# Performance work log

Measured on AMD Instinct MI355X. Metric: run time of the kernel, lower is better.

Reference implementation:

```python
import jax, jax.numpy as jnp
import numpy as np

B, S, D, H = 2, 2048, 1024, 16  # batch, seq_len, d_model(=d_k=d_v), heads
HD = D // H                      # per-head dim = 64


def setup_inputs() -> dict:
    key = jax.random.key(0)
    ks = jax.random.split(key, 7)
    s = 0.02  # weight init scale
    return {
        "queries": jax.random.normal(ks[0], (B, S, D), dtype=jnp.float32),
        "keys":    jax.random.normal(ks[1], (B, S, D), dtype=jnp.float32),
        "values":  jax.random.normal(ks[2], (B, S, D), dtype=jnp.float32),
        "Wq": jax.random.normal(ks[3], (D, D), dtype=jnp.float32) * s,
        "bq": jnp.zeros((D,), dtype=jnp.float32),
        "Wk": jax.random.normal(ks[4], (D, D), dtype=jnp.float32) * s,
        "bk": jnp.zeros((D,), dtype=jnp.float32),
        "Wv": jax.random.normal(ks[5], (D, D), dtype=jnp.float32) * s,
        "bv": jnp.zeros((D,), dtype=jnp.float32),
        "Wo": jax.random.normal(ks[6], (D, D), dtype=jnp.float32) * s,
        "bo": jnp.zeros((D,), dtype=jnp.float32),
    }


def reference(queries, keys, values, Wq, bq, Wk, bk, Wv, bv, Wo, bo):
    def split_heads(x):  # [B,S,D] -> [B,H,S,HD]
        return x.reshape(B, S, H, HD).transpose(0, 2, 1, 3)

    q = split_heads(queries @ Wq + bq)
    k = split_heads(keys @ Wk + bk)
    v = split_heads(values @ Wv + bv)

    # NOTE: original module scales by sqrt(total d_k = D), not per-head dim.
    scores = jnp.einsum('bhqd,bhkd->bhqk', q, k) / jnp.sqrt(jnp.float32(D))
    weights = jax.nn.softmax(scores, axis=-1)
    o = jnp.einsum('bhqk,bhkd->bhqd', weights, v)

    o = o.transpose(0, 2, 1, 3).reshape(B, S, D)  # merge heads
    return o @ Wo + bo
```

## Files before the change

### kernel.cpp

```cpp
#include <hip/hip_runtime.h>
#include <hip/hip_bf16.h>
#include <stdint.h>

#define S_LEN 2048
#define D_MOD 1024
#define NHEAD 16
#define BATCH 2
#define M_TOT (BATCH * S_LEN)

typedef __bf16 bf16_t;
typedef __bf16 bf16x8 __attribute__((ext_vector_type(8)));
typedef __bf16 bf16x4 __attribute__((ext_vector_type(4)));
typedef float f32x4 __attribute__((ext_vector_type(4)));

typedef __attribute__((address_space(1))) void gas_void;
typedef __attribute__((address_space(3))) void las_void;

__device__ __forceinline__ void gload_lds16(const void* g, void* l) {
#if defined(__has_builtin) && __has_builtin(__builtin_amdgcn_global_load_lds)
  __builtin_amdgcn_global_load_lds((gas_void*)g, (las_void*)l, 16u, 0, 0u);
#else
  *(bf16x8*)l = *(const bf16x8*)g;
#endif
}

__device__ __forceinline__ f32x4 mfma16(bf16x8 a, bf16x8 b, f32x4 c) {
  return __builtin_amdgcn_mfma_f32_16x16x32_bf16(a, b, c, 0, 0, 0);
}

__global__ __launch_bounds__(256) void cvt3_kernel(
    const float* __restrict__ a, const float* __restrict__ b, const float* __restrict__ c,
    bf16_t* __restrict__ oa, bf16_t* __restrict__ ob, bf16_t* __restrict__ oc)
{
  const float* in  = blockIdx.z == 0 ? a : (blockIdx.z == 1 ? b : c);
  bf16_t*      out = blockIdx.z == 0 ? oa : (blockIdx.z == 1 ? ob : oc);
  int i = blockIdx.x * 256 + threadIdx.x;
  float4 v = ((const float4*)in)[i];
  bf16x4 o;
  o[0] = (bf16_t)v.x; o[1] = (bf16_t)v.y; o[2] = (bf16_t)v.z; o[3] = (bf16_t)v.w;
  ((bf16x4*)out)[i] = o;
}

__global__ __launch_bounds__(256) void wtrans_kernel(
    const float* __restrict__ w0, const float* __restrict__ w1,
    const float* __restrict__ w2, const float* __restrict__ w3,
    bf16_t* __restrict__ t0, bf16_t* __restrict__ t1,
    bf16_t* __restrict__ t2, bf16_t* __restrict__ t3)
{
  __shared__ float tile[64][65];
  const int z = blockIdx.z;
  const float* W = z == 0 ? w0 : (z == 1 ? w1 : (z == 2 ? w2 : w3));
  bf16_t* Wt     = z == 0 ? t0 : (z == 1 ? t1 : (z == 2 ? t2 : t3));
  const int tid = threadIdx.x;
  const int kb = blockIdx.y * 64, nb = blockIdx.x * 64;
#pragma unroll
  for (int j = 0; j < 16; j++) {
    int flat = j * 256 + tid;
    int kr = flat >> 6, nc = flat & 63;
    tile[kr][nc] = W[(size_t)(kb + kr) * D_MOD + nb + nc];
  }
  __syncthreads();
#pragma unroll
  for (int j = 0; j < 16; j++) {
    int flat = j * 256 + tid;
    int nr = flat >> 6, kc = flat & 63;
    Wt[(size_t)(nb + nr) * D_MOD + kb + kc] = (bf16_t)tile[kc][nr];
  }
}

__device__ __forceinline__ void gemm_core(const bf16_t* __restrict__ A,
                                          const bf16_t* __restrict__ Bt,
                                          bf16_t* As, bf16_t* Bs,
                                          int mbase, int nbase, f32x4 acc[4][4])
{
  const int tid = threadIdx.x;
  const int lane = tid & 63, wave = tid >> 6;
  const int lrow = lane & 15, lg = lane >> 4;
  const int wm = wave >> 1, wn = wave & 1;
  for (int kt = 0; kt < D_MOD; kt += 64) {
    __syncthreads();
#pragma unroll
    for (int j = 0; j < 4; j++) {
      int flat = j * 256 + tid;
      int r = flat >> 3, c8 = flat & 7;
      gload_lds16(A  + (size_t)(mbase + r) * D_MOD + kt + c8 * 8, As + flat * 8);
      gload_lds16(Bt + (size_t)(nbase + r) * D_MOD + kt + c8 * 8, Bs + flat * 8);
    }
    __syncthreads();
#pragma unroll
    for (int kc = 0; kc < 2; kc++) {
      bf16x8 af[4], bfr[4];
#pragma unroll
      for (int mt = 0; mt < 4; mt++)
        af[mt] = *(const bf16x8*)(As + (wm * 64 + mt * 16 + lrow) * 64 + kc * 32 + lg * 8);
#pragma unroll
      for (int nt = 0; nt < 4; nt++)
        bfr[nt] = *(const bf16x8*)(Bs + (wn * 64 + nt * 16 + lrow) * 64 + kc * 32 + lg * 8);
#pragma unroll
      for (int mt = 0; mt < 4; mt++)
#pragma unroll
        for (int nt = 0; nt < 4; nt++)
          acc[mt][nt] = mfma16(af[mt], bfr[nt], acc[mt][nt]);
    }
  }
}

__global__ __launch_bounds__(256) void gemm_qkv_kernel(
    const bf16_t* __restrict__ Xq, const bf16_t* __restrict__ Xk, const bf16_t* __restrict__ Xv,
    const bf16_t* __restrict__ WqT, const bf16_t* __restrict__ WkT, const bf16_t* __restrict__ WvT,
    const float* __restrict__ bq, const float* __restrict__ bk, const float* __restrict__ bv,
    bf16_t* __restrict__ Qp, bf16_t* __restrict__ Kp, bf16_t* __restrict__ Vt)
{
  __shared__ __align__(16) bf16_t As[128 * 64];
  __shared__ __align__(16) bf16_t Bs[128 * 64];
  const int z = blockIdx.z;
  const bf16_t* A    = z == 0 ? Xq  : (z == 1 ? Xk  : Xv);
  const bf16_t* Bt   = z == 0 ? WqT : (z == 1 ? WkT : WvT);
  const float*  bias = z == 0 ? bq  : (z == 1 ? bk  : bv);
  f32x4 acc[4][4] = {};
  const int mbase = blockIdx.y * 128, nbase = blockIdx.x * 128;
  gemm_core(A, Bt, As, Bs, mbase, nbase, acc);
  const int tid = threadIdx.x, lane = tid & 63, wave = tid >> 6;
  const int lrow = lane & 15, lg = lane >> 4, wm = wave >> 1, wn = wave & 1;
  if (z < 2) {
    bf16_t* Out = z == 0 ? Qp : Kp;
#pragma unroll
    for (int mt = 0; mt < 4; mt++) {
      int r0 = mbase + wm * 64 + mt * 16 + lg * 4;
#pragma unroll
      for (int nt = 0; nt < 4; nt++) {
        int col = nbase + wn * 64 + nt * 16 + lrow;
        float bb = bias[col];
#pragma unroll
        for (int r = 0; r < 4; r++)
          Out[(size_t)(r0 + r) * D_MOD + col] = (bf16_t)(acc[mt][nt][r] + bb);
      }
    }
  } else {
#pragma unroll
    for (int mt = 0; mt < 4; mt++) {
      int r0 = mbase + wm * 64 + mt * 16 + lg * 4;
      int b = r0 >> 11, s0 = r0 & (S_LEN - 1);
#pragma unroll
      for (int nt = 0; nt < 4; nt++) {
        int col = nbase + wn * 64 + nt * 16 + lrow;
        float bb = bias[col];
        bf16x4 pk;
#pragma unroll
        for (int r = 0; r < 4; r++) pk[r] = (bf16_t)(acc[mt][nt][r] + bb);
        *(bf16x4*)(Vt + ((size_t)(b * NHEAD + (col >> 6)) * 64 + (col & 63)) * S_LEN + s0) = pk;
      }
    }
  }
}

__global__ __launch_bounds__(256) void attn_kernel(
    const bf16_t* __restrict__ Q, const bf16_t* __restrict__ K,
    const bf16_t* __restrict__ Vt, bf16_t* __restrict__ O)
{
  __shared__ __align__(16) bf16_t Ks[2][64 * 64];
  __shared__ __align__(16) bf16_t Vs[2][64 * 64];
  __shared__ __align__(16) bf16_t plds[4][32 * 72];
  const int tid = threadIdx.x, wave = tid >> 6, lane = tid & 63;
  const int lrow = lane & 15, lg = lane >> 4;
  const int bh = blockIdx.y;
  const int b = bh >> 4, h = bh & 15;
  const int qbase = blockIdx.x * 128 + wave * 32;
  const bf16_t* Kb = K + (size_t)(b * S_LEN) * D_MOD + h * 64;
  const bf16_t* Vb = Vt + (size_t)bh * 64 * S_LEN;

  bf16x8 qf[2][2];
#pragma unroll
  for (int qr = 0; qr < 2; qr++) {
    const bf16_t* Qrow = Q + (size_t)(b * S_LEN + qbase + qr * 16 + lrow) * D_MOD + h * 64;
    qf[qr][0] = *(const bf16x8*)(Qrow + lg * 8);
    qf[qr][1] = *(const bf16x8*)(Qrow + 32 + lg * 8);
  }

  float mrow[2][4], lsum[2][4];
  f32x4 oacc[2][4] = {};
#pragma unroll
  for (int qr = 0; qr < 2; qr++)
#pragma unroll
    for (int r = 0; r < 4; r++) { mrow[qr][r] = -1e30f; lsum[qr][r] = 0.f; }

  bf16_t* pl = (bf16_t*)plds[wave];
  const float sc2 = 0.03125f * 1.44269504f;
  const int rs = lrow & 7;

  auto stage = [&](int buf, int kt) {
#pragma unroll
    for (int j = 0; j < 2; j++) {
      int flat = j * 256 + tid;
      int r = flat >> 3, c8 = flat & 7;
      int sc8 = c8 ^ (r & 7);
      gload_lds16(Kb + (size_t)(kt + r) * D_MOD + sc8 * 8, &Ks[buf][flat * 8]);
    }
#pragma unroll
    for (int j = 0; j < 2; j++) {
      int flat = j * 256 + tid;
      int r = flat >> 3, c8 = flat & 7;
      int sc8 = c8 ^ (r & 7);
      gload_lds16(Vb + (size_t)r * S_LEN + kt + sc8 * 8, &Vs[buf][flat * 8]);
    }
  };

  stage(0, 0);
  __syncthreads();

  for (int kt = 0; kt < S_LEN; kt += 64) {
    const int cur = (kt >> 6) & 1;
    if (kt + 64 < S_LEN) stage(cur ^ 1, kt + 64);
    const bf16_t* Kc = Ks[cur];
    const bf16_t* Vc = Vs[cur];

    bf16x8 kf[4][2];
#pragma unroll
    for (int ct = 0; ct < 4; ct++) {
      int row = ct * 16 + lrow;
      kf[ct][0] = *(const bf16x8*)(Kc + row * 64 + ((lg) ^ rs) * 8);
      kf[ct][1] = *(const bf16x8*)(Kc + row * 64 + ((4 + lg) ^ rs) * 8);
    }
    f32x4 s[2][4] = {};
#pragma unroll
    for (int qr = 0; qr < 2; qr++)
#pragma unroll
      for (int ct = 0; ct < 4; ct++) {
        s[qr][ct] = mfma16(qf[qr][0], kf[ct][0], s[qr][ct]);
        s[qr][ct] = mfma16(qf[qr][1], kf[ct][1], s[qr][ct]);
      }

#pragma unroll
    for (int qr = 0; qr < 2; qr++) {
      float rmax[4], mn[4], corr[4], rsum[4];
#pragma unroll
      for (int r = 0; r < 4; r++)
        rmax[r] = fmaxf(fmaxf(s[qr][0][r], s[qr][1][r]), fmaxf(s[qr][2][r], s[qr][3][r]));
#pragma unroll
      for (int off = 1; off < 16; off <<= 1)
#pragma unroll
        for (int r = 0; r < 4; r++)
          rmax[r] = fmaxf(rmax[r], __shfl_xor(rmax[r], off));
#pragma unroll
      for (int r = 0; r < 4; r++) {
        mn[r] = fmaxf(mrow[qr][r], rmax[r] * sc2);
        corr[r] = __builtin_amdgcn_exp2f(mrow[qr][r] - mn[r]);
        rsum[r] = 0.f;
      }
      f32x4 p[4];
#pragma unroll
      for (int ct = 0; ct < 4; ct++)
#pragma unroll
        for (int r = 0; r < 4; r++) {
          float pv = __builtin_amdgcn_exp2f(__builtin_fmaf(s[qr][ct][r], sc2, -mn[r]));
          p[ct][r] = pv; rsum[r] += pv;
        }
#pragma unroll
      for (int off = 1; off < 16; off <<= 1)
#pragma unroll
        for (int r = 0; r < 4; r++)
          rsum[r] += __shfl_xor(rsum[r], off);
#pragma unroll
      for (int r = 0; r < 4; r++) {
        lsum[qr][r] = lsum[qr][r] * corr[r] + rsum[r];
        mrow[qr][r] = mn[r];
      }
#pragma unroll
      for (int nt = 0; nt < 4; nt++)
#pragma unroll
        for (int r = 0; r < 4; r++)
          oacc[qr][nt][r] *= corr[r];
#pragma unroll
      for (int ct = 0; ct < 4; ct++)
#pragma unroll
        for (int r = 0; r < 4; r++)
          pl[(qr * 16 + lg * 4 + r) * 72 + ct * 16 + lrow] = (bf16_t)p[ct][r];
    }

    bf16x8 vf[4][2];
#pragma unroll
    for (int nt = 0; nt < 4; nt++) {
      int row = nt * 16 + lrow;
      vf[nt][0] = *(const bf16x8*)(Vc + row * 64 + ((lg) ^ rs) * 8);
      vf[nt][1] = *(const bf16x8*)(Vc + row * 64 + ((4 + lg) ^ rs) * 8);
    }
#pragma unroll
    for (int qr = 0; qr < 2; qr++)
#pragma unroll
      for (int kc = 0; kc < 2; kc++) {
        bf16x8 af = *(const bf16x8*)(pl + (qr * 16 + lrow) * 72 + kc * 32 + lg * 8);
#pragma unroll
        for (int nt = 0; nt < 4; nt++)
          oacc[qr][nt] = mfma16(af, vf[nt][kc], oacc[qr][nt]);
      }

    __syncthreads();
  }

  bf16_t* Or = O + (size_t)(b * S_LEN + qbase) * D_MOD + h * 64;
#pragma unroll
  for (int qr = 0; qr < 2; qr++)
#pragma unroll
    for (int r = 0; r < 4; r++) {
      float inv = 1.f / lsum[qr][r];
#pragma unroll
      for (int nt = 0; nt < 4; nt++)
        Or[(size_t)(qr * 16 + lg * 4 + r) * D_MOD + nt * 16 + lrow] = (bf16_t)(oacc[qr][nt][r] * inv);
    }
}

__global__ __launch_bounds__(256) void gemm_o_kernel(
    const bf16_t* __restrict__ A, const bf16_t* __restrict__ Bt,
    const float* __restrict__ bias, float* __restrict__ Out)
{
  __shared__ __align__(16) bf16_t As[128 * 64];
  __shared__ __align__(16) bf16_t Bs[128 * 64];
  f32x4 acc[4][4] = {};
  const int mbase = blockIdx.y * 128, nbase = blockIdx.x * 128;
  gemm_core(A, Bt, As, Bs, mbase, nbase, acc);
  const int tid = threadIdx.x, lane = tid & 63, wave = tid >> 6;
  const int lrow = lane & 15, lg = lane >> 4, wm = wave >> 1, wn = wave & 1;
#pragma unroll
  for (int mt = 0; mt < 4; mt++) {
    int r0 = mbase + wm * 64 + mt * 16 + lg * 4;
#pragma unroll
    for (int nt = 0; nt < 4; nt++) {
      int col = nbase + wn * 64 + nt * 16 + lrow;
      float bb = bias[col];
#pragma unroll
      for (int r = 0; r < 4; r++)
        Out[(size_t)(r0 + r) * D_MOD + col] = acc[mt][nt][r] + bb;
    }
  }
}

extern "C" void kernel_launch(void* const* d_in, const int* in_sizes, int n_in,
                              void* d_out, int out_size, void* d_ws, size_t ws_size,
                              hipStream_t stream) {
  const float* q  = (const float*)d_in[0];
  const float* k  = (const float*)d_in[1];
  const float* v  = (const float*)d_in[2];
  const float* Wq = (const float*)d_in[3];
  const float* bq = (const float*)d_in[4];
  const float* Wk = (const float*)d_in[5];
  const float* bk = (const float*)d_in[6];
  const float* Wv = (const float*)d_in[7];
  const float* bv = (const float*)d_in[8];
  const float* Wo = (const float*)d_in[9];
  const float* bo = (const float*)d_in[10];
  float* out = (float*)d_out;

  char* ws = (char*)d_ws;
  const size_t MB = 1024 * 1024;
  bf16_t* Xq  = (bf16_t*)(ws + 0 * MB);
  bf16_t* Xk  = (bf16_t*)(ws + 8 * MB);
  bf16_t* Xv  = (bf16_t*)(ws + 16 * MB);
  bf16_t* WqT = (bf16_t*)(ws + 24 * MB);
  bf16_t* WkT = (bf16_t*)(ws + 26 * MB);
  bf16_t* WvT = (bf16_t*)(ws + 28 * MB);
  bf16_t* WoT = (bf16_t*)(ws + 30 * MB);
  bf16_t* Qp  = (bf16_t*)(ws + 32 * MB);
  bf16_t* Kp  = (bf16_t*)(ws + 40 * MB);
  bf16_t* Vt  = (bf16_t*)(ws + 48 * MB);
  bf16_t* AO  = (bf16_t*)(ws + 0 * MB);

  dim3 cb(256);
  cvt3_kernel<<<dim3(4096, 1, 3), cb, 0, stream>>>(q, k, v, Xq, Xk, Xv);
  wtrans_kernel<<<dim3(16, 16, 4), cb, 0, stream>>>(Wq, Wk, Wv, Wo, WqT, WkT, WvT, WoT);
  gemm_qkv_kernel<<<dim3(8, 32, 3), cb, 0, stream>>>(Xq, Xk, Xv, WqT, WkT, WvT,
                                                     bq, bk, bv, Qp, Kp, Vt);
  attn_kernel<<<dim3(16, 32), cb, 0, stream>>>(Qp, Kp, Vt, AO);
  gemm_o_kernel<<<dim3(8, 32), cb, 0, stream>>>(AO, WoT, bo, out);
}
```

Before: 325.9 us.

## Compute transposed S tile in flash attention to cut softmax shuffles

The QK^T MFMA operands are swapped so each lane holds a full column slice of one query row. Row max and sum then need only two cross-lane shuffles instead of four per register, and P is written to LDS as packed bf16x4 vectors instead of scalar stores. The rescale factors are redistributed to the PV accumulator layout via __shfl, and s_setprio is raised around the MFMA blocks to favor matrix issue across waves. This adds a few extra shuffles for the correction and final normalization.

```diff
diff --git a/kernel.cpp b/kernel.cpp
--- a/kernel.cpp
+++ b/kernel.cpp
@@ -177,12 +177,9 @@
     qf[qr][1] = *(const bf16x8*)(Qrow + 32 + lg * 8);
   }
 
-  float mrow[2][4], lsum[2][4];
+  float mrow[2] = {-1e30f, -1e30f};
+  float lsum[2] = {0.f, 0.f};
   f32x4 oacc[2][4] = {};
-#pragma unroll
-  for (int qr = 0; qr < 2; qr++)
-#pragma unroll
-    for (int r = 0; r < 4; r++) { mrow[qr][r] = -1e30f; lsum[qr][r] = 0.f; }
 
   bf16_t* pl = (bf16_t*)plds[wave];
   const float sc2 = 0.03125f * 1.44269504f;
@@ -221,61 +218,65 @@
       kf[ct][0] = *(const bf16x8*)(Kc + row * 64 + ((lg) ^ rs) * 8);
       kf[ct][1] = *(const bf16x8*)(Kc + row * 64 + ((4 + lg) ^ rs) * 8);
     }
-    f32x4 s[2][4] = {};
+    f32x4 st[2][4] = {};
+    __builtin_amdgcn_s_setprio(1);
 #pragma unroll
     for (int qr = 0; qr < 2; qr++)
 #pragma unroll
       for (int ct = 0; ct < 4; ct++) {
-        s[qr][ct] = mfma16(qf[qr][0], kf[ct][0], s[qr][ct]);
-        s[qr][ct] = mfma16(qf[qr][1], kf[ct][1], s[qr][ct]);
-      }
-
+        st[qr][ct] = mfma16(kf[ct][0], qf[qr][0], st[qr][ct]);
+        st[qr][ct] = mfma16(kf[ct][1], qf[qr][1], st[qr][ct]);
+      }
+    __builtin_amdgcn_s_setprio(0);
+
+    float corr_pv[2][4];
 #pragma unroll
     for (int qr = 0; qr < 2; qr++) {
-      float rmax[4], mn[4], corr[4], rsum[4];
+      f32x4 m01, m23, mm;
+#pragma unroll
+      for (int r = 0; r < 4; r++) {
+        m01[r] = fmaxf(st[qr][0][r], st[qr][1][r]);
+        m23[r] = fmaxf(st[qr][2][r], st[qr][3][r]);
+        mm[r] = fmaxf(m01[r], m23[r]);
+      }
+      float rmax = fmaxf(fmaxf(mm[0], mm[1]), fmaxf(mm[2], mm[3]));
+      rmax = fmaxf(rmax, __shfl_xor(rmax, 16));
+      rmax = fmaxf(rmax, __shfl_xor(rmax, 32));
+      float mn = fmaxf(mrow[qr], rmax * sc2);
+      float corr = __builtin_amdgcn_exp2f(mrow[qr] - mn);
+      mrow[qr] = mn;
+      f32x4 p[4];
+      f32x4 ps;
+#pragma unroll
+      for (int r = 0; r < 4; r++) {
+        p[0][r] = __builtin_amdgcn_exp2f(__builtin_fmaf(st[qr][0][r], sc2, -mn));
+        p[1][r] = __builtin_amdgcn_exp2f(__builtin_fmaf(st[qr][1][r], sc2, -mn));
+        p[2][r] = __builtin_amdgcn_exp2f(__builtin_fmaf(st[qr][2][r], sc2, -mn));
+        p[3][r] = __builtin_amdgcn_exp2f(__builtin_fmaf(st[qr][3][r], sc2, -mn));
+        ps[r] = (p[0][r] + p[1][r]) + (p[2][r] + p[3][r]);
+      }
+      float rsum = (ps[0] + ps[1]) + (ps[2] + ps[3]);
+      rsum += __shfl_xor(rsum, 16);
+      rsum += __shfl_xor(rsum, 32);
+      lsum[qr] = lsum[qr] * corr + rsum;
+#pragma unroll
+      for (int ct = 0; ct < 4; ct++) {
+        bf16x4 pk;
+#pragma unroll
+        for (int r = 0; r < 4; r++) pk[r] = (bf16_t)p[ct][r];
+        *(bf16x4*)(pl + (qr * 16 + lrow) * 72 + ct * 16 + lg * 4) = pk;
+      }
 #pragma unroll
       for (int r = 0; r < 4; r++)
-        rmax[r] = fmaxf(fmaxf(s[qr][0][r], s[qr][1][r]), fmaxf(s[qr][2][r], s[qr][3][r]));
-#pragma unroll
-      for (int off = 1; off < 16; off <<= 1)
+        corr_pv[qr][r] = __shfl(corr, lg * 4 + r);
+    }
+#pragma unroll
+    for (int qr = 0; qr < 2; qr++)
+#pragma unroll
+      for (int nt = 0; nt < 4; nt++)
 #pragma unroll
         for (int r = 0; r < 4; r++)
-          rmax[r] = fmaxf(rmax[r], __shfl_xor(rmax[r], off));
-#pragma unroll
-      for (int r = 0; r < 4; r++) {
-        mn[r] = fmaxf(mrow[qr][r], rmax[r] * sc2);
-        corr[r] = __builtin_amdgcn_exp2f(mrow[qr][r] - mn[r]);
-        rsum[r] = 0.f;
-      }
-      f32x4 p[4];
-#pragma unroll
-      for (int ct = 0; ct < 4; ct++)
-#pragma unroll
-        for (int r = 0; r < 4; r++) {
-          float pv = __builtin_amdgcn_exp2f(__builtin_fmaf(s[qr][ct][r], sc2, -mn[r]));
-          p[ct][r] = pv; rsum[r] += pv;
-        }
-#pragma unroll
-      for (int off = 1; off < 16; off <<= 1)
-#pragma unroll
-        for (int r = 0; r < 4; r++)
-          rsum[r] += __shfl_xor(rsum[r], off);
-#pragma unroll
-      for (int r = 0; r < 4; r++) {
-        lsum[qr][r] = lsum[qr][r] * corr[r] + rsum[r];
-        mrow[qr][r] = mn[r];
-      }
-#pragma unroll
-      for (int nt = 0; nt < 4; nt++)
-#pragma unroll
-        for (int r = 0; r < 4; r++)
-          oacc[qr][nt][r] *= corr[r];
-#pragma unroll
-      for (int ct = 0; ct < 4; ct++)
-#pragma unroll
-        for (int r = 0; r < 4; r++)
-          pl[(qr * 16 + lg * 4 + r) * 72 + ct * 16 + lrow] = (bf16_t)p[ct][r];
-    }
+          oacc[qr][nt][r] *= corr_pv[qr][r];
 
     bf16x8 vf[4][2];
 #pragma unroll
@@ -284,6 +285,7 @@
       vf[nt][0] = *(const bf16x8*)(Vc + row * 64 + ((lg) ^ rs) * 8);
       vf[nt][1] = *(const bf16x8*)(Vc + row * 64 + ((4 + lg) ^ rs) * 8);
     }
+    __builtin_amdgcn_s_setprio(1);
 #pragma unroll
     for (int qr = 0; qr < 2; qr++)
 #pragma unroll
@@ -293,20 +295,24 @@
         for (int nt = 0; nt < 4; nt++)
           oacc[qr][nt] = mfma16(af, vf[nt][kc], oacc[qr][nt]);
       }
+    __builtin_amdgcn_s_setprio(0);
 
     __syncthreads();
   }
 
   bf16_t* Or = O + (size_t)(b * S_LEN + qbase) * D_MOD + h * 64;
 #pragma unroll
-  for (int qr = 0; qr < 2; qr++)
-#pragma unroll
-    for (int r = 0; r < 4; r++) {
-      float inv = 1.f / lsum[qr][r];
+  for (int qr = 0; qr < 2; qr++) {
+    float linv[4];
+#pragma unroll
+    for (int r = 0; r < 4; r++)
+      linv[r] = 1.f / __shfl(lsum[qr], lg * 4 + r);
+#pragma unroll
+    for (int r = 0; r < 4; r++)
 #pragma unroll
       for (int nt = 0; nt < 4; nt++)
-        Or[(size_t)(qr * 16 + lg * 4 + r) * D_MOD + nt * 16 + lrow] = (bf16_t)(oacc[qr][nt][r] * inv);
-    }
+        Or[(size_t)(qr * 16 + lg * 4 + r) * D_MOD + nt * 16 + lrow] = (bf16_t)(oacc[qr][nt][r] * linv[r]);
+  }
 }
 
 __global__ __launch_bounds__(256) void gemm_o_kernel(
```

After: 269.1 us. -17.4%, faster.
